# Kernel tuning notes

Measured on AMD Instinct MI355X. Metric: run time of the kernel, lower is better.

The kernel has to match this reference:

```python
import jax, jax.numpy as jnp
import numpy as np

B, S, D, H, FB, K, FC = 16, 512, 256, 8, 128, 64, 32


def setup_inputs() -> dict:
    key = jax.random.key(0)
    ks = jax.random.split(key, 16)
    g = lambda i, shp: jax.random.normal(ks[i], shp, dtype=jnp.float32)
    inp = {
        "B_target": g(0, (B, S, FB)),
        "B_infected": g(1, (B, S, FB)),
        "E_target": g(2, (B, S, D)),
        "E_infected": g(3, (B, S, D)),
        "C_target": jax.random.uniform(ks[4], (B, S, K, FC), dtype=jnp.float32),
        "C_infected": jax.random.uniform(ks[5], (B, S, K, FC), dtype=jnp.float32),
        # learned parameters
        "W_bs": g(6, (FB, 1)) * 0.1,
        "W_cs": g(7, (FC, 1)) * 0.1,
        "W1": g(8, (H, D, D)) * (1.0 / np.sqrt(D)),  # per-head Attn W1, batched
        "W2": g(9, (H, D, D)) * (1.0 / np.sqrt(D)),
        "gamma_bs": jnp.ones((S,), jnp.float32),
        "beta_bs": jnp.zeros((S,), jnp.float32),
        "gamma_cs": jnp.ones((S,), jnp.float32),
        "beta_cs": jnp.zeros((S,), jnp.float32),
        "W_f": g(10, (2, 1)) * 0.1,
    }
    return inp


def _weighted_sum(x, W):
    # tf.nn.softmax over trailing size-1 axis of [F,1] -> all ones (faithful)
    return jnp.squeeze(x @ jax.nn.softmax(W, axis=-1), -1)


def _l2norm(x):
    return x * jax.lax.rsqrt(jnp.maximum(jnp.sum(x * x, -1, keepdims=True), 1e-12))


def _layernorm(x, gamma, beta, eps=1e-16):
    m = jnp.mean(x, -1, keepdims=True)
    v = jnp.mean(jnp.square(x - m), -1, keepdims=True)
    return (x - m) * jax.lax.rsqrt(v + eps) * gamma + beta


def _kld(y_true, y_pred, eps=1e-7):
    yt = jnp.clip(y_true, eps, 1.0)
    yp = jnp.clip(y_pred, eps, 1.0)
    return jnp.sum(yt * jnp.log(yt / yp), -1)


def _attn_br(Bvec, E, W1, W2):
    # batched multi-head version of the per-head Attn loop
    Q = jnp.einsum('bsd,hde->bhse', E, W1)
    Kh = jnp.einsum('bsd,hde->bhse', E, W2)
    scale = 1.0 / jnp.sqrt(jnp.asarray(E.shape[-1], E.dtype))
    scores = jnp.einsum('bhse,bhte->bhst', Q, Kh) * scale  # [b,H,S,S]
    A = jax.nn.softmax(scores, axis=2)  # original softmax(axis=1) on [b,S,S]
    # Dot(axes=(1,1)) of [b,S] with [b,S,S] -> [b,S]; stack heads, transpose -> [b,S,H]
    return jnp.einsum('bs,bhst->bth', Bvec, A)


def reference(B_target, B_infected, E_target, E_infected, C_target, C_infected,
              W_bs, W_cs, W1, W2, gamma_bs, beta_bs, gamma_cs, beta_cs, W_f):
    Bt = _weighted_sum(B_target, W_bs)   # [b,S]
    Bi = _weighted_sum(B_infected, W_bs)
    BR_t = _attn_br(Bt, E_target, W1, W2)    # [b,S,H]
    BR_i = _attn_br(Bi, E_infected, W1, W2)
    # keras CosineSimilarity loss = -cos_sim
    cos = -jnp.sum(_l2norm(BR_i) * _l2norm(BR_t), -1)  # [b,S]
    BS_out = _layernorm(cos, gamma_bs, beta_bs)
    Ct = _weighted_sum(C_target, W_cs)   # [b,S,K]
    Ci = _weighted_sum(C_infected, W_cs)
    Cm = 0.5 * (Ct + Ci)
    Cv = 0.5 * _kld(Ci, Cm) + 0.5 * _kld(Ct, Cm)  # [b,S]
    CS_out = _layernorm(Cv, gamma_cs, beta_cs)
    composite = jnp.stack([BS_out, CS_out], axis=-1)  # [b,S,2]
    out = jnp.squeeze(composite @ jax.nn.softmax(W_f, axis=-1), -1)
    return (out, BS_out, CS_out)
```

## Files before the change

kernel.cpp:

```cpp
#include <hip/hip_runtime.h>

#define NB 16
#define NS 512
#define ND 256
#define NH 8
#define NFB 128
#define NK 64
#define NFC 32

using f16 = _Float16;
using f16x4 = __attribute__((ext_vector_type(4))) f16;
using f16x8 = __attribute__((ext_vector_type(8))) f16;
using f32x4 = __attribute__((ext_vector_type(4))) float;

__device__ inline float waveReduceSum(float v) {
    #pragma unroll
    for (int off = 32; off; off >>= 1) v += __shfl_down(v, off);
    return v;
}

__device__ inline f32x4 mfma16(f16x8 a, f16x8 b, f32x4 c) {
    return __builtin_amdgcn_mfma_f32_16x16x32_f16(a, b, c, 0, 0, 0);
}

__global__ __launch_bounds__(256) void k_convert(const float* __restrict__ Et, const float* __restrict__ Ei,
                                                 f16* __restrict__ Ot, f16* __restrict__ Oi) {
    const int n4 = NB * NS * ND / 4;
    int i = blockIdx.x * 256 + threadIdx.x;
    const float* src; f16* dst;
    if (i < n4) { src = Et; dst = Ot; }
    else        { src = Ei; dst = Oi; i -= n4; }
    float4 v = ((const float4*)src)[i];
    f16x4 o = { (f16)v.x, (f16)v.y, (f16)v.z, (f16)v.w };
    ((f16x4*)dst)[i] = o;
}

__global__ __launch_bounds__(256) void k_bsum(const float* __restrict__ Bt_in, const float* __restrict__ Bi_in,
                                              float* __restrict__ Bt, float* __restrict__ Bi) {
    int wid = (blockIdx.x * 256 + threadIdx.x) >> 6;
    int lane = threadIdx.x & 63;
    const float* src; float* dst; int row;
    if (wid < NB * NS) { src = Bt_in; dst = Bt; row = wid; }
    else               { src = Bi_in; dst = Bi; row = wid - NB * NS; }
    float2 v = ((const float2*)(src + (size_t)row * NFB))[lane];
    float s = waveReduceSum(v.x + v.y);
    if (lane == 0) dst[row] = s;
}

__global__ __launch_bounds__(256) void k_cv(const float* __restrict__ Ct, const float* __restrict__ Ci,
                                            float* __restrict__ Cv) {
    int gw = (blockIdx.x * 256 + threadIdx.x) >> 6;
    int lane = threadIdx.x & 63;
    const float* pt = Ct + ((size_t)gw * NK + lane) * NFC;
    const float* pi = Ci + ((size_t)gw * NK + lane) * NFC;
    float st = 0.f, si = 0.f;
    #pragma unroll
    for (int j = 0; j < NFC; j += 4) {
        float4 vt = *(const float4*)(pt + j); st += vt.x + vt.y + vt.z + vt.w;
        float4 vi = *(const float4*)(pi + j); si += vi.x + vi.y + vi.z + vi.w;
    }
    float cm = 0.5f * (st + si);
    float yp = fminf(fmaxf(cm, 1e-7f), 1.0f);
    float y1 = fminf(fmaxf(si, 1e-7f), 1.0f);
    float y2 = fminf(fmaxf(st, 1e-7f), 1.0f);
    float term = 0.5f * (y1 * logf(y1 / yp) + y2 * logf(y2 / yp));
    term = waveReduceSum(term);
    if (lane == 0) Cv[gw] = term;
}

__global__ __launch_bounds__(256) void k_mt(const float* __restrict__ W1, const float* __restrict__ W2,
                                            f16* __restrict__ Mth) {
    int h  = blockIdx.x >> 4;
    int j0 = ((blockIdx.x >> 2) & 3) * 64;
    int i0 = (blockIdx.x & 3) * 64;
    const float* A  = W2 + (size_t)h * ND * ND;
    const float* Bm = W1 + (size_t)h * ND * ND;
    __shared__ float Wa[64][36];
    __shared__ float Wb[64][36];
    int tid = threadIdx.x;
    int r = tid >> 4, c = tid & 15;
    float acc[4][4] = {};
    for (int d0 = 0; d0 < ND; d0 += 32) {
        __syncthreads();
        #pragma unroll
        for (int i = 0; i < 2; ++i) {
            int sid = tid + i * 256;
            int row = sid >> 3, seg = sid & 7;
            *(float4*)&Wa[row][seg * 4] = *(const float4*)&A [(size_t)(j0 + row) * ND + d0 + seg * 4];
            *(float4*)&Wb[row][seg * 4] = *(const float4*)&Bm[(size_t)(i0 + row) * ND + d0 + seg * 4];
        }
        __syncthreads();
        #pragma unroll 8
        for (int d = 0; d < 32; ++d) {
            float a0 = Wa[r*4+0][d], a1 = Wa[r*4+1][d], a2 = Wa[r*4+2][d], a3 = Wa[r*4+3][d];
            float b0 = Wb[c*4+0][d], b1 = Wb[c*4+1][d], b2 = Wb[c*4+2][d], b3 = Wb[c*4+3][d];
            acc[0][0] += a0*b0; acc[0][1] += a0*b1; acc[0][2] += a0*b2; acc[0][3] += a0*b3;
            acc[1][0] += a1*b0; acc[1][1] += a1*b1; acc[1][2] += a1*b2; acc[1][3] += a1*b3;
            acc[2][0] += a2*b0; acc[2][1] += a2*b1; acc[2][2] += a2*b2; acc[2][3] += a2*b3;
            acc[3][0] += a3*b0; acc[3][1] += a3*b1; acc[3][2] += a3*b2; acc[3][3] += a3*b3;
        }
    }
    #pragma unroll
    for (int a = 0; a < 4; ++a)
        #pragma unroll
        for (int bb = 0; bb < 4; ++bb)
            Mth[(size_t)h * ND * ND + (size_t)(j0 + r * 4 + a) * ND + (i0 + c * 4 + bb)] = (f16)acc[a][bb];
}

__global__ __launch_bounds__(256) void k_pgemm(const f16* __restrict__ Eft, const f16* __restrict__ Efi,
                                               const f16* __restrict__ Mth,
                                               f16* __restrict__ Pt, f16* __restrict__ Pi) {
    int idx = blockIdx.x;
    const f16* E; f16* P;
    if (idx < 1024) { E = Eft; P = Pt; }
    else            { idx -= 1024; E = Efi; P = Pi; }
    int bh = idx >> 3, b = bh >> 3, h = bh & 7;
    int t = idx & 7;
    int m0 = (t >> 1) * 128, n0 = (t & 1) * 128;
    const f16* A  = E + (size_t)b * NS * ND;
    const f16* Bm = Mth + (size_t)h * ND * ND;
    f16* C = P + (size_t)bh * NS * ND;

    __shared__ f16 As[128 * 40];
    __shared__ f16 Bs[128 * 40];

    int tid = threadIdx.x;
    int lane = tid & 63, w = tid >> 6;
    int wm = (w >> 1) * 64, wn = (w & 1) * 64;
    int l16 = lane & 15, ch = lane >> 4;

    f32x4 acc[4][4] = {};

    for (int k0 = 0; k0 < ND; k0 += 32) {
        __syncthreads();
        #pragma unroll
        for (int i = 0; i < 2; ++i) {
            int sid = tid + i * 256;
            int row = sid >> 2, seg = sid & 3;
            *(int4*)&As[row * 40 + seg * 8] = *(const int4*)&A [(size_t)(m0 + row) * ND + k0 + seg * 8];
            *(int4*)&Bs[row * 40 + seg * 8] = *(const int4*)&Bm[(size_t)(n0 + row) * ND + k0 + seg * 8];
        }
        __syncthreads();
        f16x8 a[4], bb[4];
        #pragma unroll
        for (int mi = 0; mi < 4; ++mi) a[mi]  = *(const f16x8*)&As[(wm + mi * 16 + l16) * 40 + ch * 8];
        #pragma unroll
        for (int ni = 0; ni < 4; ++ni) bb[ni] = *(const f16x8*)&Bs[(wn + ni * 16 + l16) * 40 + ch * 8];
        #pragma unroll
        for (int mi = 0; mi < 4; ++mi)
            #pragma unroll
            for (int ni = 0; ni < 4; ++ni)
                acc[mi][ni] = mfma16(a[mi], bb[ni], acc[mi][ni]);
    }
    #pragma unroll
    for (int mi = 0; mi < 4; ++mi)
        #pragma unroll
        for (int ni = 0; ni < 4; ++ni) {
            int col = n0 + wn + ni * 16 + l16;
            int rbase = m0 + wm + mi * 16 + ch * 4;
            #pragma unroll
            for (int r = 0; r < 4; ++r)
                C[(size_t)(rbase + r) * ND + col] = (f16)acc[mi][ni][r];
        }
}

__global__ __launch_bounds__(256, 3) void k_attn2(const f16* __restrict__ Pt, const f16* __restrict__ Pi,
                                                  const f16* __restrict__ Eft, const f16* __restrict__ Efi,
                                                  const float* __restrict__ Bst, const float* __restrict__ Bsi,
                                                  float* __restrict__ PEt, float* __restrict__ PBt,
                                                  float* __restrict__ PEi, float* __restrict__ PBi) {
    int x = blockIdx.x;
    const f16 *P, *E; const float* Bvg; float *PE, *PB;
    if (x < 512) { P = Pt; E = Eft; Bvg = Bst; PE = PEt; PB = PBt; }
    else         { x -= 512; P = Pi; E = Efi; Bvg = Bsi; PE = PEi; PB = PBi; }
    int b = x >> 5, h = (x >> 2) & 7, st = x & 3;
    int s0 = st * 128;
    const f16* Pbase = P + ((size_t)(b * NH + h) * NS + s0) * ND;
    const f16* Ebase = E + (size_t)b * NS * ND;
    float* PEo = PE + (size_t)(b * NH + h) * NS;
    float* PBo = PB + (size_t)(b * NH + h) * NS;

    __shared__ f16 Et[64 * 264];
    __shared__ float pe_s[NS], pb_s[NS];

    int tid = threadIdx.x;
    int lane = tid & 63, w = tid >> 6;
    int l16 = lane & 15, ch = lane >> 4;

    pe_s[tid] = 0.f; pe_s[tid + 256] = 0.f;
    pb_s[tid] = 0.f; pb_s[tid + 256] = 0.f;

    f16x8 af[2][8];
    #pragma unroll
    for (int mt = 0; mt < 2; ++mt)
        #pragma unroll
        for (int kk = 0; kk < 8; ++kk)
            af[mt][kk] = *(const f16x8*)&Pbase[(size_t)(w * 32 + mt * 16 + l16) * ND + kk * 32 + ch * 8];

    float bvr[2][4];
    #pragma unroll
    for (int mt = 0; mt < 2; ++mt)
        #pragma unroll
        for (int r = 0; r < 4; ++r)
            bvr[mt][r] = Bvg[b * NS + s0 + w * 32 + mt * 16 + ch * 4 + r];

    for (int t0 = 0; t0 < NS; t0 += 64) {
        __syncthreads();
        #pragma unroll
        for (int i = 0; i < 8; ++i) {
            int sid = tid + i * 256;
            int row = sid >> 5, seg = sid & 31;
            *(int4*)&Et[row * 264 + seg * 8] = *(const int4*)&Ebase[(size_t)(t0 + row) * ND + seg * 8];
        }
        __syncthreads();
        f32x4 sacc[2][4] = {};
        #pragma unroll
        for (int kk = 0; kk < 8; ++kk)
            #pragma unroll
            for (int nt = 0; nt < 4; ++nt) {
                f16x8 bf = *(const f16x8*)&Et[(nt * 16 + l16) * 264 + kk * 32 + ch * 8];
                sacc[0][nt] = mfma16(af[0][kk], bf, sacc[0][nt]);
                sacc[1][nt] = mfma16(af[1][kk], bf, sacc[1][nt]);
            }
        #pragma unroll
        for (int nt = 0; nt < 4; ++nt) {
            float se = 0.f, sw = 0.f;
            #pragma unroll
            for (int mt = 0; mt < 2; ++mt)
                #pragma unroll
                for (int r = 0; r < 4; ++r) {
                    float e = __expf(sacc[mt][nt][r] * 0.0625f);
                    se += e; sw += bvr[mt][r] * e;
                }
            se += __shfl_down(se, 32); se += __shfl_down(se, 16);
            sw += __shfl_down(sw, 32); sw += __shfl_down(sw, 16);
            if (ch == 0) {
                atomicAdd(&pe_s[t0 + nt * 16 + l16], se);
                atomicAdd(&pb_s[t0 + nt * 16 + l16], sw);
            }
        }
    }
    __syncthreads();
    atomicAdd(&PEo[tid],       pe_s[tid]);
    atomicAdd(&PEo[tid + 256], pe_s[tid + 256]);
    atomicAdd(&PBo[tid],       pb_s[tid]);
    atomicAdd(&PBo[tid + 256], pb_s[tid + 256]);
}

__device__ inline float blockSum512(float v, float* rbuf) {
    v = waveReduceSum(v);
    int lane = threadIdx.x & 63, w = threadIdx.x >> 6;
    __syncthreads();
    if (lane == 0) rbuf[w] = v;
    __syncthreads();
    float s = 0.f;
    #pragma unroll
    for (int i = 0; i < 8; ++i) s += rbuf[i];
    return s;
}

__global__ __launch_bounds__(512) void k_final(const float* __restrict__ PEt, const float* __restrict__ PBt,
                                               const float* __restrict__ PEi, const float* __restrict__ PBi,
                                               const float* __restrict__ Cv,
                                               const float* __restrict__ gbs, const float* __restrict__ bbs,
                                               const float* __restrict__ gcs, const float* __restrict__ bcs,
                                               float* __restrict__ out) {
    __shared__ float rbuf[8];
    int b = blockIdx.x, s = threadIdx.x;
    float dot = 0.f, nt = 0.f, nu = 0.f;
    #pragma unroll
    for (int h = 0; h < NH; ++h) {
        size_t idx = (size_t)(b * NH + h) * NS + s;
        float tv = PBt[idx] / PEt[idx];
        float iv = PBi[idx] / PEi[idx];
        dot += tv * iv; nt += tv * tv; nu += iv * iv;
    }
    float cosv = -(dot * rsqrtf(fmaxf(nt, 1e-12f)) * rsqrtf(fmaxf(nu, 1e-12f)));

    float mc = blockSum512(cosv, rbuf) * (1.f / 512.f);
    float dc = cosv - mc;
    float vc = blockSum512(dc * dc, rbuf) * (1.f / 512.f);
    float BS = dc * rsqrtf(vc + 1e-16f) * gbs[s] + bbs[s];

    float cv = Cv[(size_t)b * NS + s];
    float mv = blockSum512(cv, rbuf) * (1.f / 512.f);
    float dv = cv - mv;
    float vv = blockSum512(dv * dv, rbuf) * (1.f / 512.f);
    float CS = dv * rsqrtf(vv + 1e-16f) * gcs[s] + bcs[s];

    out[(size_t)b * NS + s] = BS + CS;
    out[(size_t)NB * NS + (size_t)b * NS + s] = BS;
    out[(size_t)2 * NB * NS + (size_t)b * NS + s] = CS;
}

extern "C" void kernel_launch(void* const* d_in, const int* in_sizes, int n_in,
                              void* d_out, int out_size, void* d_ws, size_t ws_size,
                              hipStream_t stream) {
    const float* B_target   = (const float*)d_in[0];
    const float* B_infected = (const float*)d_in[1];
    const float* E_target   = (const float*)d_in[2];
    const float* E_infected = (const float*)d_in[3];
    const float* C_target   = (const float*)d_in[4];
    const float* C_infected = (const float*)d_in[5];
    const float* W1  = (const float*)d_in[8];
    const float* W2  = (const float*)d_in[9];
    const float* gbs = (const float*)d_in[10];
    const float* bbs = (const float*)d_in[11];
    const float* gcs = (const float*)d_in[12];
    const float* bcs = (const float*)d_in[13];
    float* out = (float*)d_out;

    char* ws = (char*)d_ws;
    size_t off = 0;
    auto alloc = [&](size_t n) { char* p = ws + off; off = (off + n + 255) & ~(size_t)255; return p; };
    float* Bt  = (float*)alloc((size_t)NB * NS * 4);
    float* Bi  = (float*)alloc((size_t)NB * NS * 4);
    float* Cv  = (float*)alloc((size_t)NB * NS * 4);
    float* PEt = (float*)alloc((size_t)NB * NH * NS * 4);
    float* PBt = (float*)alloc((size_t)NB * NH * NS * 4);
    float* PEi = (float*)alloc((size_t)NB * NH * NS * 4);
    float* PBi = (float*)alloc((size_t)NB * NH * NS * 4);
    f16* Mth = (f16*)alloc((size_t)NH * ND * ND * 2);
    f16* Eft = (f16*)alloc((size_t)NB * NS * ND * 2);
    f16* Efi = (f16*)alloc((size_t)NB * NS * ND * 2);
    f16* Pt  = (f16*)alloc((size_t)NB * NH * NS * ND * 2);
    f16* Pi  = (f16*)alloc((size_t)NB * NH * NS * ND * 2);

    hipMemsetAsync(PEt, 0, (size_t)4 * NB * NH * NS * 4, stream);
    k_convert<<<4096, 256, 0, stream>>>(E_target, E_infected, Eft, Efi);
    k_bsum<<<4096, 256, 0, stream>>>(B_target, B_infected, Bt, Bi);
    k_cv<<<2048, 256, 0, stream>>>(C_target, C_infected, Cv);
    k_mt<<<128, 256, 0, stream>>>(W1, W2, Mth);
    k_pgemm<<<2048, 256, 0, stream>>>(Eft, Efi, Mth, Pt, Pi);
    k_attn2<<<1024, 256, 0, stream>>>(Pt, Pi, Eft, Efi, Bt, Bi, PEt, PBt, PEi, PBi);
    k_final<<<NB, 512, 0, stream>>>(PEt, PBt, PEi, PBi, Cv, gbs, bbs, gcs, bcs, out);
}
```

Baseline: 327.1 us.

## Fuse projection GEMM into attention kernel and merge prep kernels into one launch

Removes the intermediate P = E·M^T tensor (B*H*S*D fp16 per side, written and re-read through global memory) by computing each wave's projected rows in registers inside the attention kernel, staging M tiles through shared memory. The four small preprocessing kernels (weight product, fp16 conversion, B sums, C divergence) are merged into one launch dispatched on block index. The attention loop now reads E key tiles straight from global/L2 with split f16x4 loads instead of staging them in shared memory. This trades a large memory round trip and several launches for extra per-block recompute and possibly less coalesced, cache-dependent key loads.

```diff
diff --git a/kernel.cpp b/kernel.cpp
--- a/kernel.cpp
+++ b/kernel.cpp
@@ -23,164 +23,108 @@
     return __builtin_amdgcn_mfma_f32_16x16x32_f16(a, b, c, 0, 0, 0);
 }
 
-__global__ __launch_bounds__(256) void k_convert(const float* __restrict__ Et, const float* __restrict__ Ei,
-                                                 f16* __restrict__ Ot, f16* __restrict__ Oi) {
-    const int n4 = NB * NS * ND / 4;
-    int i = blockIdx.x * 256 + threadIdx.x;
-    const float* src; f16* dst;
-    if (i < n4) { src = Et; dst = Ot; }
-    else        { src = Ei; dst = Oi; i -= n4; }
-    float4 v = ((const float4*)src)[i];
-    f16x4 o = { (f16)v.x, (f16)v.y, (f16)v.z, (f16)v.w };
-    ((f16x4*)dst)[i] = o;
-}
-
-__global__ __launch_bounds__(256) void k_bsum(const float* __restrict__ Bt_in, const float* __restrict__ Bi_in,
-                                              float* __restrict__ Bt, float* __restrict__ Bi) {
-    int wid = (blockIdx.x * 256 + threadIdx.x) >> 6;
-    int lane = threadIdx.x & 63;
-    const float* src; float* dst; int row;
-    if (wid < NB * NS) { src = Bt_in; dst = Bt; row = wid; }
-    else               { src = Bi_in; dst = Bi; row = wid - NB * NS; }
-    float2 v = ((const float2*)(src + (size_t)row * NFB))[lane];
-    float s = waveReduceSum(v.x + v.y);
-    if (lane == 0) dst[row] = s;
-}
-
-__global__ __launch_bounds__(256) void k_cv(const float* __restrict__ Ct, const float* __restrict__ Ci,
-                                            float* __restrict__ Cv) {
-    int gw = (blockIdx.x * 256 + threadIdx.x) >> 6;
-    int lane = threadIdx.x & 63;
-    const float* pt = Ct + ((size_t)gw * NK + lane) * NFC;
-    const float* pi = Ci + ((size_t)gw * NK + lane) * NFC;
-    float st = 0.f, si = 0.f;
-    #pragma unroll
-    for (int j = 0; j < NFC; j += 4) {
-        float4 vt = *(const float4*)(pt + j); st += vt.x + vt.y + vt.z + vt.w;
-        float4 vi = *(const float4*)(pi + j); si += vi.x + vi.y + vi.z + vi.w;
-    }
-    float cm = 0.5f * (st + si);
-    float yp = fminf(fmaxf(cm, 1e-7f), 1.0f);
-    float y1 = fminf(fmaxf(si, 1e-7f), 1.0f);
-    float y2 = fminf(fmaxf(st, 1e-7f), 1.0f);
-    float term = 0.5f * (y1 * logf(y1 / yp) + y2 * logf(y2 / yp));
-    term = waveReduceSum(term);
-    if (lane == 0) Cv[gw] = term;
-}
-
-__global__ __launch_bounds__(256) void k_mt(const float* __restrict__ W1, const float* __restrict__ W2,
-                                            f16* __restrict__ Mth) {
-    int h  = blockIdx.x >> 4;
-    int j0 = ((blockIdx.x >> 2) & 3) * 64;
-    int i0 = (blockIdx.x & 3) * 64;
-    const float* A  = W2 + (size_t)h * ND * ND;
-    const float* Bm = W1 + (size_t)h * ND * ND;
+__global__ __launch_bounds__(256) void k_prep(const float* __restrict__ W1, const float* __restrict__ W2,
+                                              f16* __restrict__ Mth,
+                                              const float* __restrict__ Et_in, const float* __restrict__ Ei_in,
+                                              f16* __restrict__ Ot, f16* __restrict__ Oi,
+                                              const float* __restrict__ Bt_in, const float* __restrict__ Bi_in,
+                                              float* __restrict__ Bt, float* __restrict__ Bi,
+                                              const float* __restrict__ Ct, const float* __restrict__ Ci,
+                                              float* __restrict__ Cv) {
     __shared__ float Wa[64][36];
     __shared__ float Wb[64][36];
+    int bid = blockIdx.x;
     int tid = threadIdx.x;
-    int r = tid >> 4, c = tid & 15;
-    float acc[4][4] = {};
-    for (int d0 = 0; d0 < ND; d0 += 32) {
-        __syncthreads();
-        #pragma unroll
-        for (int i = 0; i < 2; ++i) {
-            int sid = tid + i * 256;
-            int row = sid >> 3, seg = sid & 7;
-            *(float4*)&Wa[row][seg * 4] = *(const float4*)&A [(size_t)(j0 + row) * ND + d0 + seg * 4];
-            *(float4*)&Wb[row][seg * 4] = *(const float4*)&Bm[(size_t)(i0 + row) * ND + d0 + seg * 4];
-        }
-        __syncthreads();
-        #pragma unroll 8
-        for (int d = 0; d < 32; ++d) {
-            float a0 = Wa[r*4+0][d], a1 = Wa[r*4+1][d], a2 = Wa[r*4+2][d], a3 = Wa[r*4+3][d];
-            float b0 = Wb[c*4+0][d], b1 = Wb[c*4+1][d], b2 = Wb[c*4+2][d], b3 = Wb[c*4+3][d];
-            acc[0][0] += a0*b0; acc[0][1] += a0*b1; acc[0][2] += a0*b2; acc[0][3] += a0*b3;
-            acc[1][0] += a1*b0; acc[1][1] += a1*b1; acc[1][2] += a1*b2; acc[1][3] += a1*b3;
-            acc[2][0] += a2*b0; acc[2][1] += a2*b1; acc[2][2] += a2*b2; acc[2][3] += a2*b3;
-            acc[3][0] += a3*b0; acc[3][1] += a3*b1; acc[3][2] += a3*b2; acc[3][3] += a3*b3;
-        }
+
+    if (bid < 128) {
+        int h  = bid >> 4;
+        int j0 = ((bid >> 2) & 3) * 64;
+        int i0 = (bid & 3) * 64;
+        const float* A  = W2 + (size_t)h * ND * ND;
+        const float* Bm = W1 + (size_t)h * ND * ND;
+        int r = tid >> 4, c = tid & 15;
+        float acc[4][4] = {};
+        for (int d0 = 0; d0 < ND; d0 += 32) {
+            __syncthreads();
+            #pragma unroll
+            for (int i = 0; i < 2; ++i) {
+                int sid = tid + i * 256;
+                int row = sid >> 3, seg = sid & 7;
+                *(float4*)&Wa[row][seg * 4] = *(const float4*)&A [(size_t)(j0 + row) * ND + d0 + seg * 4];
+                *(float4*)&Wb[row][seg * 4] = *(const float4*)&Bm[(size_t)(i0 + row) * ND + d0 + seg * 4];
+            }
+            __syncthreads();
+            #pragma unroll 8
+            for (int d = 0; d < 32; ++d) {
+                float a0 = Wa[r*4+0][d], a1 = Wa[r*4+1][d], a2 = Wa[r*4+2][d], a3 = Wa[r*4+3][d];
+                float b0 = Wb[c*4+0][d], b1 = Wb[c*4+1][d], b2 = Wb[c*4+2][d], b3 = Wb[c*4+3][d];
+                acc[0][0] += a0*b0; acc[0][1] += a0*b1; acc[0][2] += a0*b2; acc[0][3] += a0*b3;
+                acc[1][0] += a1*b0; acc[1][1] += a1*b1; acc[1][2] += a1*b2; acc[1][3] += a1*b3;
+                acc[2][0] += a2*b0; acc[2][1] += a2*b1; acc[2][2] += a2*b2; acc[2][3] += a2*b3;
+                acc[3][0] += a3*b0; acc[3][1] += a3*b1; acc[3][2] += a3*b2; acc[3][3] += a3*b3;
+            }
+        }
+        #pragma unroll
+        for (int a = 0; a < 4; ++a)
+            #pragma unroll
+            for (int bb = 0; bb < 4; ++bb)
+                Mth[(size_t)h * ND * ND + (size_t)(j0 + r * 4 + a) * ND + (i0 + c * 4 + bb)] = (f16)acc[a][bb];
+    } else if (bid < 128 + 4096) {
+        const int n4 = NB * NS * ND / 4;
+        int i = (bid - 128) * 256 + tid;
+        const float* src; f16* dst;
+        if (i < n4) { src = Et_in; dst = Ot; }
+        else        { src = Ei_in; dst = Oi; i -= n4; }
+        float4 v = ((const float4*)src)[i];
+        f16x4 o = { (f16)v.x, (f16)v.y, (f16)v.z, (f16)v.w };
+        ((f16x4*)dst)[i] = o;
+    } else if (bid < 128 + 8192) {
+        int wid = ((bid - 128 - 4096) * 256 + tid) >> 6;
+        int lane = tid & 63;
+        const float* src; float* dst; int row;
+        if (wid < NB * NS) { src = Bt_in; dst = Bt; row = wid; }
+        else               { src = Bi_in; dst = Bi; row = wid - NB * NS; }
+        float2 v = ((const float2*)(src + (size_t)row * NFB))[lane];
+        float s = waveReduceSum(v.x + v.y);
+        if (lane == 0) dst[row] = s;
+    } else {
+        int gw = ((bid - 128 - 8192) * 256 + tid) >> 6;
+        int lane = tid & 63;
+        const float* pt = Ct + ((size_t)gw * NK + lane) * NFC;
+        const float* pi = Ci + ((size_t)gw * NK + lane) * NFC;
+        float st = 0.f, si = 0.f;
+        #pragma unroll
+        for (int j = 0; j < NFC; j += 4) {
+            float4 vt = *(const float4*)(pt + j); st += vt.x + vt.y + vt.z + vt.w;
+            float4 vi = *(const float4*)(pi + j); si += vi.x + vi.y + vi.z + vi.w;
+        }
+        float cm = 0.5f * (st + si);
+        float yp = fminf(fmaxf(cm, 1e-7f), 1.0f);
+        float y1 = fminf(fmaxf(si, 1e-7f), 1.0f);
+        float y2 = fminf(fmaxf(st, 1e-7f), 1.0f);
+        float term = 0.5f * (y1 * logf(y1 / yp) + y2 * logf(y2 / yp));
+        term = waveReduceSum(term);
+        if (lane == 0) Cv[gw] = term;
     }
-    #pragma unroll
-    for (int a = 0; a < 4; ++a)
-        #pragma unroll
-        for (int bb = 0; bb < 4; ++bb)
-            Mth[(size_t)h * ND * ND + (size_t)(j0 + r * 4 + a) * ND + (i0 + c * 4 + bb)] = (f16)acc[a][bb];
-}
-
-__global__ __launch_bounds__(256) void k_pgemm(const f16* __restrict__ Eft, const f16* __restrict__ Efi,
-                                               const f16* __restrict__ Mth,
-                                               f16* __restrict__ Pt, f16* __restrict__ Pi) {
-    int idx = blockIdx.x;
-    const f16* E; f16* P;
-    if (idx < 1024) { E = Eft; P = Pt; }
-    else            { idx -= 1024; E = Efi; P = Pi; }
-    int bh = idx >> 3, b = bh >> 3, h = bh & 7;
-    int t = idx & 7;
-    int m0 = (t >> 1) * 128, n0 = (t & 1) * 128;
-    const f16* A  = E + (size_t)b * NS * ND;
-    const f16* Bm = Mth + (size_t)h * ND * ND;
-    f16* C = P + (size_t)bh * NS * ND;
-
-    __shared__ f16 As[128 * 40];
-    __shared__ f16 Bs[128 * 40];
-
-    int tid = threadIdx.x;
-    int lane = tid & 63, w = tid >> 6;
-    int wm = (w >> 1) * 64, wn = (w & 1) * 64;
-    int l16 = lane & 15, ch = lane >> 4;
-
-    f32x4 acc[4][4] = {};
-
-    for (int k0 = 0; k0 < ND; k0 += 32) {
-        __syncthreads();
-        #pragma unroll
-        for (int i = 0; i < 2; ++i) {
-            int sid = tid + i * 256;
-            int row = sid >> 2, seg = sid & 3;
-            *(int4*)&As[row * 40 + seg * 8] = *(const int4*)&A [(size_t)(m0 + row) * ND + k0 + seg * 8];
-            *(int4*)&Bs[row * 40 + seg * 8] = *(const int4*)&Bm[(size_t)(n0 + row) * ND + k0 + seg * 8];
-        }
-        __syncthreads();
-        f16x8 a[4], bb[4];
-        #pragma unroll
-        for (int mi = 0; mi < 4; ++mi) a[mi]  = *(const f16x8*)&As[(wm + mi * 16 + l16) * 40 + ch * 8];
-        #pragma unroll
-        for (int ni = 0; ni < 4; ++ni) bb[ni] = *(const f16x8*)&Bs[(wn + ni * 16 + l16) * 40 + ch * 8];
-        #pragma unroll
-        for (int mi = 0; mi < 4; ++mi)
-            #pragma unroll
-            for (int ni = 0; ni < 4; ++ni)
-                acc[mi][ni] = mfma16(a[mi], bb[ni], acc[mi][ni]);
-    }
-    #pragma unroll
-    for (int mi = 0; mi < 4; ++mi)
-        #pragma unroll
-        for (int ni = 0; ni < 4; ++ni) {
-            int col = n0 + wn + ni * 16 + l16;
-            int rbase = m0 + wm + mi * 16 + ch * 4;
-            #pragma unroll
-            for (int r = 0; r < 4; ++r)
-                C[(size_t)(rbase + r) * ND + col] = (f16)acc[mi][ni][r];
-        }
-}
-
-__global__ __launch_bounds__(256, 3) void k_attn2(const f16* __restrict__ Pt, const f16* __restrict__ Pi,
-                                                  const f16* __restrict__ Eft, const f16* __restrict__ Efi,
+}
+
+__global__ __launch_bounds__(256, 3) void k_attn3(const f16* __restrict__ Eft, const f16* __restrict__ Efi,
+                                                  const f16* __restrict__ Mth,
                                                   const float* __restrict__ Bst, const float* __restrict__ Bsi,
                                                   float* __restrict__ PEt, float* __restrict__ PBt,
                                                   float* __restrict__ PEi, float* __restrict__ PBi) {
     int x = blockIdx.x;
-    const f16 *P, *E; const float* Bvg; float *PE, *PB;
-    if (x < 512) { P = Pt; E = Eft; Bvg = Bst; PE = PEt; PB = PBt; }
-    else         { x -= 512; P = Pi; E = Efi; Bvg = Bsi; PE = PEi; PB = PBi; }
-    int b = x >> 5, h = (x >> 2) & 7, st = x & 3;
-    int s0 = st * 128;
-    const f16* Pbase = P + ((size_t)(b * NH + h) * NS + s0) * ND;
+    const f16* E; const float* Bvg; float *PE, *PB;
+    if (x < 512) { E = Eft; Bvg = Bst; PE = PEt; PB = PBt; }
+    else         { x -= 512; E = Efi; Bvg = Bsi; PE = PEi; PB = PBi; }
+    int b = x >> 5, h = (x >> 2) & 7;
+    int s0 = (x & 3) * 128;
     const f16* Ebase = E + (size_t)b * NS * ND;
+    const f16* Mh = Mth + (size_t)h * ND * ND;
     float* PEo = PE + (size_t)(b * NH + h) * NS;
     float* PBo = PB + (size_t)(b * NH + h) * NS;
 
-    __shared__ f16 Et[64 * 264];
+    __shared__ f16 Ms[32 * 264];
     __shared__ float pe_s[NS], pb_s[NS];
 
     int tid = threadIdx.x;
@@ -190,35 +134,61 @@
     pe_s[tid] = 0.f; pe_s[tid + 256] = 0.f;
     pb_s[tid] = 0.f; pb_s[tid + 256] = 0.f;
 
+    int sw0 = s0 + w * 32;
+
+    f16x8 ebf[2][8];
+    #pragma unroll
+    for (int st = 0; st < 2; ++st)
+        #pragma unroll
+        for (int ki = 0; ki < 8; ++ki)
+            ebf[st][ki] = *(const f16x8*)&Ebase[(size_t)(sw0 + st * 16 + l16) * ND + ki * 32 + ch * 8];
+
+    float bvr[2][4];
+    #pragma unroll
+    for (int st = 0; st < 2; ++st)
+        #pragma unroll
+        for (int r = 0; r < 4; ++r)
+            bvr[st][r] = Bvg[b * NS + sw0 + st * 16 + 4 * ch + r];
+
     f16x8 af[2][8];
-    #pragma unroll
-    for (int mt = 0; mt < 2; ++mt)
+    for (int jc = 0; jc < 8; ++jc) {
+        __syncthreads();
+        #pragma unroll
+        for (int it = 0; it < 4; ++it) {
+            int sid = tid + it * 256;
+            int row = sid >> 5, seg = sid & 31;
+            *(int4*)&Ms[row * 264 + seg * 8] = *(const int4*)&Mh[(size_t)(jc * 32 + row) * ND + seg * 8];
+        }
+        __syncthreads();
+        f32x4 acc[2][2] = {};
+        #pragma unroll
+        for (int ki = 0; ki < 8; ++ki) {
+            f16x8 a0 = *(const f16x8*)&Ms[(l16)      * 264 + ki * 32 + ch * 8];
+            f16x8 a1 = *(const f16x8*)&Ms[(16 + l16) * 264 + ki * 32 + ch * 8];
+            acc[0][0] = mfma16(a0, ebf[0][ki], acc[0][0]);
+            acc[0][1] = mfma16(a0, ebf[1][ki], acc[0][1]);
+            acc[1][0] = mfma16(a1, ebf[0][ki], acc[1][0]);
+            acc[1][1] = mfma16(a1, ebf[1][ki], acc[1][1]);
+        }
+        #pragma unroll
+        for (int st = 0; st < 2; ++st) {
+            f16x8 v;
+            #pragma unroll
+            for (int r = 0; r < 4; ++r) { v[r] = (f16)acc[0][st][r]; v[4 + r] = (f16)acc[1][st][r]; }
+            af[st][jc] = v;
+        }
+    }
+
+    for (int t0 = 0; t0 < NS; t0 += 64) {
+        f32x4 sacc[2][4] = {};
         #pragma unroll
         for (int kk = 0; kk < 8; ++kk)
-            af[mt][kk] = *(const f16x8*)&Pbase[(size_t)(w * 32 + mt * 16 + l16) * ND + kk * 32 + ch * 8];
-
-    float bvr[2][4];
-    #pragma unroll
-    for (int mt = 0; mt < 2; ++mt)
-        #pragma unroll
-        for (int r = 0; r < 4; ++r)
-            bvr[mt][r] = Bvg[b * NS + s0 + w * 32 + mt * 16 + ch * 4 + r];
-
-    for (int t0 = 0; t0 < NS; t0 += 64) {
-        __syncthreads();
-        #pragma unroll
-        for (int i = 0; i < 8; ++i) {
-            int sid = tid + i * 256;
-            int row = sid >> 5, seg = sid & 31;
-            *(int4*)&Et[row * 264 + seg * 8] = *(const int4*)&Ebase[(size_t)(t0 + row) * ND + seg * 8];
-        }
-        __syncthreads();
-        f32x4 sacc[2][4] = {};
-        #pragma unroll
-        for (int kk = 0; kk < 8; ++kk)
             #pragma unroll
             for (int nt = 0; nt < 4; ++nt) {
-                f16x8 bf = *(const f16x8*)&Et[(nt * 16 + l16) * 264 + kk * 32 + ch * 8];
+                const f16* ep = &Ebase[(size_t)(t0 + nt * 16 + l16) * ND + kk * 32 + 4 * ch];
+                f16x4 lo = *(const f16x4*)ep;
+                f16x4 hi = *(const f16x4*)(ep + 16);
+                f16x8 bf = { lo[0], lo[1], lo[2], lo[3], hi[0], hi[1], hi[2], hi[3] };
                 sacc[0][nt] = mfma16(af[0][kk], bf, sacc[0][nt]);
                 sacc[1][nt] = mfma16(af[1][kk], bf, sacc[1][nt]);
             }
@@ -226,11 +196,11 @@
         for (int nt = 0; nt < 4; ++nt) {
             float se = 0.f, sw = 0.f;
             #pragma unroll
-            for (int mt = 0; mt < 2; ++mt)
+            for (int st = 0; st < 2; ++st)
                 #pragma unroll
                 for (int r = 0; r < 4; ++r) {
-                    float e = __expf(sacc[mt][nt][r] * 0.0625f);
-                    se += e; sw += bvr[mt][r] * e;
+                    float e = __expf(sacc[st][nt][r] * 0.0625f);
+                    se += e; sw += bvr[st][r] * e;
                 }
             se += __shfl_down(se, 32); se += __shfl_down(se, 16);
             sw += __shfl_down(sw, 32); sw += __shfl_down(sw, 16);
@@ -323,15 +293,12 @@
     f16* Mth = (f16*)alloc((size_t)NH * ND * ND * 2);
     f16* Eft = (f16*)alloc((size_t)NB * NS * ND * 2);
     f16* Efi = (f16*)alloc((size_t)NB * NS * ND * 2);
-    f16* Pt  = (f16*)alloc((size_t)NB * NH * NS * ND * 2);
-    f16* Pi  = (f16*)alloc((size_t)NB * NH * NS * ND * 2);
 
     hipMemsetAsync(PEt, 0, (size_t)4 * NB * NH * NS * 4, stream);
-    k_convert<<<4096, 256, 0, stream>>>(E_target, E_infected, Eft, Efi);
-    k_bsum<<<4096, 256, 0, stream>>>(B_target, B_infected, Bt, Bi);
-    k_cv<<<2048, 256, 0, stream>>>(C_target, C_infected, Cv);
-    k_mt<<<128, 256, 0, stream>>>(W1, W2, Mth);
-    k_pgemm<<<2048, 256, 0, stream>>>(Eft, Efi, Mth, Pt, Pi);
-    k_attn2<<<1024, 256, 0, stream>>>(Pt, Pi, Eft, Efi, Bt, Bi, PEt, PBt, PEi, PBi);
+    k_prep<<<128 + 8192 + 2048, 256, 0, stream>>>(W1, W2, Mth,
+                                                  E_target, E_infected, Eft, Efi,
+                                                  B_target, B_infected, Bt, Bi,
+                                                  C_target, C_infected, Cv);
+    k_attn3<<<1024, 256, 0, stream>>>(Eft, Efi, Mth, Bt, Bi, PEt, PBt, PEi, PBi);
     k_final<<<NB, 512, 0, stream>>>(PEt, PBt, PEi, PBi, Cv, gbs, bbs, gcs, bcs, out);
 }
```

Result: slower. 498.7 us (+52.5%).
